# Performance work log

Measured on AMD Instinct MI355X. Metric: run time of the kernel, lower is better.

The kernel has to match this reference:

```python
import jax, jax.numpy as jnp
import numpy as np

V, D, DEPTH, L, H, DH, FF = 32000, 1024, 4, 2048, 16, 64, 4096
INNER = H * DH
EPS = 1e-5


def ln(x, g, b):
    m = jnp.mean(x, axis=-1, keepdims=True)
    v = jnp.mean(jnp.square(x - m), axis=-1, keepdims=True)
    return (x - m) * jax.lax.rsqrt(v + EPS) * g + b


def setup_inputs() -> dict:
    key = jax.random.key(0)
    ks = jax.random.split(key, 16)
    s = 0.02
    inp = {
        'x': jax.random.randint(ks[0], (1, L), 0, V),
        'tok_emb': jax.random.normal(ks[1], (V, D), jnp.float32) * s,
        'pos_emb': jax.random.normal(ks[2], (L, D), jnp.float32) * s,
        'attn_ng': jnp.ones((DEPTH, D), jnp.float32),
        'attn_nb': jnp.zeros((DEPTH, D), jnp.float32),
        'wqkv': jax.random.normal(ks[3], (DEPTH, D, 3 * INNER), jnp.float32) * s,
        'wo': jax.random.normal(ks[4], (DEPTH, INNER, D), jnp.float32) * s,
        'bo': jnp.zeros((DEPTH, D), jnp.float32),
        'out_ng': jnp.ones((DEPTH, D), jnp.float32),
        'out_nb': jnp.zeros((DEPTH, D), jnp.float32),
        'ff_ng': jnp.ones((DEPTH, D), jnp.float32),
        'ff_nb': jnp.zeros((DEPTH, D), jnp.float32),
        'w1': jax.random.normal(ks[5], (DEPTH, D, FF), jnp.float32) * s,
        'b1': jnp.zeros((DEPTH, FF), jnp.float32),
        'w2': jax.random.normal(ks[6], (DEPTH, FF, D), jnp.float32) * s,
        'b2': jnp.zeros((DEPTH, D), jnp.float32),
        'fin_g': jnp.ones((D,), jnp.float32),
        'fin_b': jnp.zeros((D,), jnp.float32),
        'w_logit': jax.random.normal(ks[7], (D, V), jnp.float32) * s,
        'b_logit': jnp.zeros((V,), jnp.float32),
    }
    return inp


def reference(x, tok_emb, pos_emb, attn_ng, attn_nb, wqkv, wo, bo, out_ng, out_nb,
              ff_ng, ff_nb, w1, b1, w2, b2, fin_g, fin_b, w_logit, b_logit):
    n = x.shape[1]
    scale = DH ** -0.5
    # causal keep-mask: j <= i (lower triangular incl diagonal)
    causal = jnp.tril(jnp.ones((n, n), bool))
    h = tok_emb[x] + pos_emb[:n][None]  # [b, n, D]
    for l in range(DEPTH):
        # --- ReLA attention ---
        y = ln(h, attn_ng[l], attn_nb[l])
        qkv = y @ wqkv[l]  # [b, n, 3*INNER]
        q, k, v = jnp.split(qkv, 3, axis=-1)
        q = q.reshape(-1, n, H, DH).transpose(0, 2, 1, 3) * scale  # [b,H,n,d]
        k = k.reshape(-1, n, H, DH).transpose(0, 2, 1, 3)
        v = v.reshape(-1, n, H, DH).transpose(0, 2, 1, 3)
        sim = jnp.einsum('bhid,bhjd->bhij', q, k)
        attn = jnp.where(causal, jax.nn.relu(sim), 0.0)  # mask then ReLU
        o = jnp.einsum('bhij,bhjd->bhid', attn, v)
        o = o.transpose(0, 2, 1, 3).reshape(-1, n, INNER)  # [b,n,INNER]
        o = ln(o @ wo[l] + bo[l], out_ng[l], out_nb[l])
        h = o + h
        # --- FFN ---
        y = ln(h, ff_ng[l], ff_nb[l])
        y = jax.nn.gelu(y @ w1[l] + b1[l], approximate=False) @ w2[l] + b2[l]
        h = y + h
    return ln(h, fin_g, fin_b) @ w_logit + b_logit
```

## Files before the change

kernel.cpp:

```cpp
#include <hip/hip_runtime.h>
#include <hip/hip_bf16.h>
#include <math.h>

#define SEQ   2048
#define DM    1024
#define NH    16
#define DHD   64
#define FFD   4096
#define NV    32000

typedef __bf16 bf16x8 __attribute__((ext_vector_type(8)));
typedef float  f32x4  __attribute__((ext_vector_type(4)));

typedef __attribute__((address_space(1))) void* gas_ptr;
typedef __attribute__((address_space(3))) void* las_ptr;

static __device__ __forceinline__ void gload16(const void* g, void* l) {
  __builtin_amdgcn_global_load_lds((gas_ptr)g, (las_ptr)l, 16, 0, 0);
}

static __device__ __forceinline__ unsigned short f2bf(float f) {
  unsigned int x = __float_as_uint(f);
  return (unsigned short)((x + 0x7fffu + ((x >> 16) & 1u)) >> 16);
}

static __device__ __forceinline__ bf16x8 ld_frag(const unsigned short* p) {
  union { uint4 u; bf16x8 v; } r;
  r.u = *(const uint4*)p;
  return r.v;
}

__global__ __launch_bounds__(256)
void k_transpose_bf16(const float* __restrict__ in, unsigned short* __restrict__ out,
                      int K, int N, size_t lstride) {
  in  += (size_t)blockIdx.z * lstride;
  out += (size_t)blockIdx.z * lstride;
  __shared__ float tl[64 * 65];
  const int bk = blockIdx.x * 64, bn = blockIdx.y * 64;
  const int t = threadIdx.x;
  const int tx = t & 15, ty = t >> 4;
#pragma unroll
  for (int i = 0; i < 4; ++i) {
    const int r = i * 16 + ty;
    float4 v = *(const float4*)&in[(size_t)(bk + r) * N + bn + tx * 4];
    tl[(tx * 4 + 0) * 65 + r] = v.x;
    tl[(tx * 4 + 1) * 65 + r] = v.y;
    tl[(tx * 4 + 2) * 65 + r] = v.z;
    tl[(tx * 4 + 3) * 65 + r] = v.w;
  }
  __syncthreads();
#pragma unroll
  for (int j = 0; j < 2; ++j) {
    const int f = j * 256 + t;
    const int n = f >> 3, kc = (f & 7) * 8;
    union { unsigned short u[8]; uint4 v; } pk;
#pragma unroll
    for (int e = 0; e < 8; ++e) pk.u[e] = f2bf(tl[n * 65 + kc + e]);
    *(uint4*)&out[(size_t)(bn + n) * K + bk + kc] = pk.v;
  }
}

__global__ __launch_bounds__(256)
void k_vT(const unsigned short* __restrict__ qkv, unsigned short* __restrict__ vT) {
  __shared__ unsigned short tile[32][33];
  const int bs = blockIdx.x * 32, bd = blockIdx.y * 32;
  const int tx = threadIdx.x & 31, ty = threadIdx.x >> 5;
#pragma unroll
  for (int r = ty; r < 32; r += 8)
    tile[r][tx] = qkv[(size_t)(bs + r) * (3 * DM) + 2 * DM + bd + tx];
  __syncthreads();
#pragma unroll
  for (int r = ty; r < 32; r += 8)
    vT[(size_t)(bd + r) * SEQ + bs + tx] = tile[tx][r];
}

__global__ __launch_bounds__(256)
void k_embed(const int* __restrict__ x, const float* __restrict__ tok,
             const float* __restrict__ pos, float* __restrict__ h) {
  const int row = blockIdx.x;
  const int d = threadIdx.x * 4;
  const int tk = x[row];
  float4 a = *(const float4*)(tok + (size_t)tk * DM + d);
  float4 p = *(const float4*)(pos + (size_t)row * DM + d);
  float4 o; o.x = a.x + p.x; o.y = a.y + p.y; o.z = a.z + p.z; o.w = a.w + p.w;
  *(float4*)(h + (size_t)row * DM + d) = o;
}

__global__ __launch_bounds__(256)
void k_ln_bf16(const float* __restrict__ in, const float* __restrict__ g,
               const float* __restrict__ b, unsigned short* __restrict__ out) {
  const int row = blockIdx.x, t = threadIdx.x;
  float4 v = *(const float4*)(in + (size_t)row * DM + t * 4);
  float s = v.x + v.y + v.z + v.w;
  float q = v.x * v.x + v.y * v.y + v.z * v.z + v.w * v.w;
#pragma unroll
  for (int o = 32; o; o >>= 1) { s += __shfl_xor(s, o); q += __shfl_xor(q, o); }
  __shared__ float ls[4], lq[4];
  if ((t & 63) == 0) { ls[t >> 6] = s; lq[t >> 6] = q; }
  __syncthreads();
  s = ls[0] + ls[1] + ls[2] + ls[3];
  q = lq[0] + lq[1] + lq[2] + lq[3];
  const float mean = s * (1.f / DM);
  const float rstd = rsqrtf(q * (1.f / DM) - mean * mean + 1e-5f);
  float4 gg = *(const float4*)(g + t * 4);
  float4 bb = *(const float4*)(b + t * 4);
  ushort4 o4;
  o4.x = f2bf((v.x - mean) * rstd * gg.x + bb.x);
  o4.y = f2bf((v.y - mean) * rstd * gg.y + bb.y);
  o4.z = f2bf((v.z - mean) * rstd * gg.z + bb.z);
  o4.w = f2bf((v.w - mean) * rstd * gg.w + bb.w);
  *(ushort4*)(out + (size_t)row * DM + t * 4) = o4;
}

__global__ __launch_bounds__(256)
void k_add_ln_ln(float* __restrict__ h, const float* __restrict__ in,
                 const float* __restrict__ g1, const float* __restrict__ b1,
                 const float* __restrict__ g2, const float* __restrict__ b2,
                 unsigned short* __restrict__ out) {
  const int row = blockIdx.x, t = threadIdx.x;
  __shared__ float ls[4], lq[4], ls2[4], lq2[4];
  float4 v = *(const float4*)(in + (size_t)row * DM + t * 4);
  float s = v.x + v.y + v.z + v.w;
  float q = v.x * v.x + v.y * v.y + v.z * v.z + v.w * v.w;
#pragma unroll
  for (int o = 32; o; o >>= 1) { s += __shfl_xor(s, o); q += __shfl_xor(q, o); }
  if ((t & 63) == 0) { ls[t >> 6] = s; lq[t >> 6] = q; }
  __syncthreads();
  s = ls[0] + ls[1] + ls[2] + ls[3];
  q = lq[0] + lq[1] + lq[2] + lq[3];
  const float mean = s * (1.f / DM);
  const float rstd = rsqrtf(q * (1.f / DM) - mean * mean + 1e-5f);
  float4 gg = *(const float4*)(g1 + t * 4);
  float4 bb = *(const float4*)(b1 + t * 4);
  float4 hv = *(const float4*)(h + (size_t)row * DM + t * 4);
  hv.x += (v.x - mean) * rstd * gg.x + bb.x;
  hv.y += (v.y - mean) * rstd * gg.y + bb.y;
  hv.z += (v.z - mean) * rstd * gg.z + bb.z;
  hv.w += (v.w - mean) * rstd * gg.w + bb.w;
  *(float4*)(h + (size_t)row * DM + t * 4) = hv;
  float s2 = hv.x + hv.y + hv.z + hv.w;
  float q2 = hv.x * hv.x + hv.y * hv.y + hv.z * hv.z + hv.w * hv.w;
#pragma unroll
  for (int o = 32; o; o >>= 1) { s2 += __shfl_xor(s2, o); q2 += __shfl_xor(q2, o); }
  if ((t & 63) == 0) { ls2[t >> 6] = s2; lq2[t >> 6] = q2; }
  __syncthreads();
  s2 = ls2[0] + ls2[1] + ls2[2] + ls2[3];
  q2 = lq2[0] + lq2[1] + lq2[2] + lq2[3];
  const float mean2 = s2 * (1.f / DM);
  const float rstd2 = rsqrtf(q2 * (1.f / DM) - mean2 * mean2 + 1e-5f);
  float4 g2v = *(const float4*)(g2 + t * 4);
  float4 b2v = *(const float4*)(b2 + t * 4);
  ushort4 o4;
  o4.x = f2bf((hv.x - mean2) * rstd2 * g2v.x + b2v.x);
  o4.y = f2bf((hv.y - mean2) * rstd2 * g2v.y + b2v.y);
  o4.z = f2bf((hv.z - mean2) * rstd2 * g2v.z + b2v.z);
  o4.w = f2bf((hv.w - mean2) * rstd2 * g2v.w + b2v.w);
  *(ushort4*)(out + (size_t)row * DM + t * 4) = o4;
}

__global__ __launch_bounds__(256)
void k_red_add(float* __restrict__ h, const float* __restrict__ sl,
               const float* __restrict__ b2) {
  const int row = blockIdx.x, d = threadIdx.x * 4;
  const size_t idx = (size_t)row * DM + d;
  float4 hv = *(const float4*)(h + idx);
  float4 bb = *(const float4*)(b2 + d);
  hv.x += bb.x; hv.y += bb.y; hv.z += bb.z; hv.w += bb.w;
#pragma unroll
  for (int c = 0; c < 4; ++c) {
    float4 p = *(const float4*)(sl + (size_t)c * SEQ * DM + idx);
    hv.x += p.x; hv.y += p.y; hv.z += p.z; hv.w += p.w;
  }
  *(float4*)(h + idx) = hv;
}

template<int EPI>
__global__ __launch_bounds__(512, 1)
void k_gemm2(const unsigned short* __restrict__ A, const unsigned short* __restrict__ Bt,
             float* __restrict__ outF, unsigned short* __restrict__ outB,
             const float* __restrict__ bias, int N, int K, int kLen, int gm) {
  __shared__ __align__(16) unsigned short L[49152];
  const int nwg = gridDim.x, pid = blockIdx.x;
  const int qq = nwg >> 3, rr = nwg & 7;
  const int xcd = pid & 7, lo = pid >> 3;
  const int wg = ((xcd < rr) ? xcd * (qq + 1) : rr * (qq + 1) + (xcd - rr) * qq) + lo;
  const int bm = wg % gm, bn = wg / gm;
  const int kOff = blockIdx.y * kLen;
  const int t = threadIdx.x, lane = t & 63, w = t >> 6;
  const int wm = w >> 2, wn = w & 3, lr = lane & 15, lg = lane >> 4;

  const unsigned short* gA[2]; unsigned short* lA[2];
  const unsigned short* gB[4]; unsigned short* lB[4];
#pragma unroll
  for (int j = 0; j < 2; ++j) {
    const int f = j * 512 + t, row = f >> 3, c = f & 7;
    gA[j] = A + (size_t)(bm * 128 + row) * K + kOff + ((c ^ (row & 7)) << 3);
    lA[j] = L + f * 8;
  }
#pragma unroll
  for (int j = 0; j < 4; ++j) {
    const int f = j * 512 + t, row = f >> 3, c = f & 7;
    gB[j] = Bt + (size_t)(bn * 256 + row) * K + kOff + ((c ^ (row & 7)) << 3);
    lB[j] = L + 16384 + f * 8;
  }
  auto stage = [&](int k0, int c) {
#pragma unroll
    for (int j = 0; j < 2; ++j) gload16(gA[j] + k0, lA[j] + c * 8192);
#pragma unroll
    for (int j = 0; j < 4; ++j) gload16(gB[j] + k0, lB[j] + c * 16384);
  };

  int offA[4][2], offB[4][2];
#pragma unroll
  for (int mt = 0; mt < 4; ++mt)
#pragma unroll
    for (int ks = 0; ks < 2; ++ks) {
      const int rowA = wm * 64 + mt * 16 + lr;
      offA[mt][ks] = rowA * 64 + (((ks * 4 + lg) ^ (rowA & 7)) << 3);
      const int rowB = wn * 64 + mt * 16 + lr;
      offB[mt][ks] = rowB * 64 + (((ks * 4 + lg) ^ (rowB & 7)) << 3);
    }

  const f32x4 zero = {0.f, 0.f, 0.f, 0.f};
  f32x4 acc[4][4];
#pragma unroll
  for (int i = 0; i < 4; ++i)
#pragma unroll
    for (int j = 0; j < 4; ++j) acc[i][j] = zero;

  const int NT = kLen >> 6;
  stage(0, 0);
  if (NT > 1) stage(64, 1);

  for (int tt = 0; tt < NT; ++tt) {
    const int c = tt & 1;
    if (tt + 1 < NT) asm volatile("s_waitcnt vmcnt(6)" ::: "memory");
    else             asm volatile("s_waitcnt vmcnt(0)" ::: "memory");
    __builtin_amdgcn_s_barrier();
    const unsigned short* Ab = L + c * 8192;
    const unsigned short* Bb = L + 16384 + c * 16384;
    bf16x8 af[4][2], bfr[4][2];
#pragma unroll
    for (int mt = 0; mt < 4; ++mt)
#pragma unroll
      for (int ks = 0; ks < 2; ++ks) {
        af[mt][ks]  = ld_frag(Ab + offA[mt][ks]);
        bfr[mt][ks] = ld_frag(Bb + offB[mt][ks]);
      }
    __builtin_amdgcn_s_setprio(1);
#pragma unroll
    for (int mt = 0; mt < 4; ++mt)
#pragma unroll
      for (int nt = 0; nt < 4; ++nt)
#pragma unroll
        for (int ks = 0; ks < 2; ++ks)
          acc[mt][nt] = __builtin_amdgcn_mfma_f32_16x16x32_bf16(af[mt][ks], bfr[nt][ks], acc[mt][nt], 0, 0, 0);
    __builtin_amdgcn_s_setprio(0);
    asm volatile("s_waitcnt lgkmcnt(0)" ::: "memory");
    __builtin_amdgcn_s_barrier();
    if (tt + 2 < NT) stage((tt + 2) << 6, c);
  }

  const int rbase = bm * 128 + wm * 64;
  const int cbase = bn * 256 + wn * 64;
  float* outP = outF;
  if constexpr (EPI == 4) outP = outF + (size_t)blockIdx.y * SEQ * N;
#pragma unroll
  for (int mt = 0; mt < 4; ++mt) {
#pragma unroll
    for (int nt = 0; nt < 4; ++nt) {
      const int col = cbase + nt * 16 + lr;
      float bv = 0.f;
      if constexpr (EPI == 1 || EPI == 2) bv = bias[col];
#pragma unroll
      for (int r = 0; r < 4; ++r) {
        const int row = rbase + mt * 16 + lg * 4 + r;
        float v = acc[mt][nt][r] + bv;
        if constexpr (EPI == 2) v = 0.5f * v * (1.f + erff(v * 0.70710678118f));
        if constexpr (EPI == 0 || EPI == 2) outB[(size_t)row * N + col] = f2bf(v);
        else                                outP[(size_t)row * N + col] = v;
      }
    }
  }
}

__global__ __launch_bounds__(512, 1)
void k_gemm3(const unsigned short* __restrict__ A, const unsigned short* __restrict__ Bt,
             float* __restrict__ outF, const float* __restrict__ bias,
             int N, int K, int gm) {
  __shared__ __align__(16) unsigned short L[65536];
  const int nwg = gridDim.x, pid = blockIdx.x;
  const int qq = nwg >> 3, rr = nwg & 7;
  const int xcd = pid & 7, lo = pid >> 3;
  const int wg = ((xcd < rr) ? xcd * (qq + 1) : rr * (qq + 1) + (xcd - rr) * qq) + lo;
  const int bm = wg % gm, bn = wg / gm;
  const int t = threadIdx.x, lane = t & 63, w = t >> 6;
  const int wm = w >> 2, wn = w & 3, lr = lane & 15, lg = lane >> 4;
  const int NT = K >> 6;

  int offA[8][2], offB[4][2];
#pragma unroll
  for (int mt = 0; mt < 8; ++mt) {
    const int row = mt * 32 + wm * 16 + lr;
#pragma unroll
    for (int ks = 0; ks < 2; ++ks)
      offA[mt][ks] = row * 64 + (((ks * 4 + lg) ^ (row & 7)) << 3);
  }
#pragma unroll
  for (int nt = 0; nt < 4; ++nt) {
    const int row = ((nt & 1) << 6) + ((nt >> 1) << 7) + wn * 16 + lr;
#pragma unroll
    for (int ks = 0; ks < 2; ++ks)
      offB[nt][ks] = 16384 + row * 64 + (((ks * 4 + lg) ^ (row & 7)) << 3);
  }

  const unsigned short* gA = A  + (size_t)(bm * 256) * K;
  const unsigned short* gB = Bt + (size_t)(bn * 256) * K;

  auto stage_half = [&](int which, int tile, int half) {
    const int tt = (tile < NT) ? tile : (NT - 1);
    const unsigned short* g = which ? gB : gA;
    const int bufo = (tile & 1) << 15;
#pragma unroll
    for (int j = 0; j < 2; ++j) {
      const int f = (j << 9) + t;
      const int r = (half << 7) + (f >> 3);
      const int c = (f & 7) ^ (r & 7);
      gload16(g + (size_t)r * K + (tt << 6) + (c << 3),
              L + bufo + (which << 14) + (half << 13) + f * 8);
    }
  };

  f32x4 acc[8][4];
#pragma unroll
  for (int i = 0; i < 8; ++i)
#pragma unroll
    for (int j = 0; j < 4; ++j) acc[i][j] = (f32x4){0.f, 0.f, 0.f, 0.f};
  bf16x8 af[4][2], bfr[2][2];

  stage_half(1, 0, 0); stage_half(0, 0, 1); stage_half(0, 0, 0);
  stage_half(1, 0, 1); stage_half(1, 1, 0); stage_half(0, 1, 1);

#define PHASE(VMS, LDA, LDB, MH, NH, BUFO, SW, ST, SH) do {                    \
  asm volatile("s_waitcnt vmcnt(" VMS ")" ::: "memory");                       \
  __builtin_amdgcn_s_barrier();                                                \
  if (LDA) {                                                                   \
    _Pragma("unroll") for (int mt = 0; mt < 4; ++mt)                           \
    _Pragma("unroll") for (int ks = 0; ks < 2; ++ks)                           \
      af[mt][ks] = ld_frag(L + (BUFO) + offA[(MH) * 4 + mt][ks]);              \
  }                                                                            \
  if (LDB) {                                                                   \
    _Pragma("unroll") for (int n = 0; n < 2; ++n)                              \
    _Pragma("unroll") for (int ks = 0; ks < 2; ++ks)                           \
      bfr[n][ks] = ld_frag(L + (BUFO) + offB[(NH) * 2 + n][ks]);               \
  }                                                                            \
  stage_half((SW), (ST), (SH));                                                \
  asm volatile("s_waitcnt lgkmcnt(0)" ::: "memory");                           \
  __builtin_amdgcn_sched_barrier(0);                                           \
  __builtin_amdgcn_s_setprio(1);                                               \
  _Pragma("unroll") for (int mt = 0; mt < 4; ++mt)                             \
  _Pragma("unroll") for (int n = 0; n < 2; ++n)                                \
  _Pragma("unroll") for (int ks = 0; ks < 2; ++ks)                             \
    acc[(MH) * 4 + mt][(NH) * 2 + n] = __builtin_amdgcn_mfma_f32_16x16x32_bf16(\
        af[mt][ks], bfr[n][ks], acc[(MH) * 4 + mt][(NH) * 2 + n], 0, 0, 0);    \
  __builtin_amdgcn_s_setprio(0);                                               \
} while (0)

  for (int I = 0; I < (NT >> 1); ++I) {
    const int T = I << 1;
    PHASE("4", 1, 1, 0, 0, 0,     0, T + 1, 0);
    PHASE("8", 1, 0, 1, 0, 0,     1, T + 1, 1);
    PHASE("6", 0, 1, 1, 1, 0,     1, T + 2, 0);
    PHASE("8", 1, 0, 0, 1, 0,     0, T + 2, 1);
    PHASE("4", 1, 1, 0, 0, 32768, 0, T + 2, 0);
    PHASE("8", 1, 0, 1, 0, 32768, 1, T + 2, 1);
    PHASE("6", 0, 1, 1, 1, 32768, 1, T + 3, 0);
    PHASE("8", 1, 0, 0, 1, 32768, 0, T + 3, 1);
  }
#undef PHASE

#pragma unroll
  for (int mt = 0; mt < 8; ++mt) {
    const int row0 = bm * 256 + mt * 32 + wm * 16 + lg * 4;
#pragma unroll
    for (int nt = 0; nt < 4; ++nt) {
      const int col = bn * 256 + ((nt & 1) << 6) + ((nt >> 1) << 7) + wn * 16 + lr;
      const float bv = bias[col];
#pragma unroll
      for (int r = 0; r < 4; ++r)
        outF[(size_t)(row0 + r) * N + col] = acc[mt][nt][r] + bv;
    }
  }
}

__global__ __launch_bounds__(256)
void k_rela_attn(const unsigned short* __restrict__ qkv,
                 const unsigned short* __restrict__ vT,
                 unsigned short* __restrict__ obf) {
  const int jb = blockIdx.x;
  const int hd = blockIdx.y;
  const int qbA = jb, qbB = 31 - jb;
  const int t = threadIdx.x, lane = t & 63, w = t >> 6;
  const int lr = lane & 15, lg = lane >> 4;

  __shared__ __align__(16) unsigned short Qs[128 * 64];
  __shared__ __align__(16) unsigned short Ks[64 * 64];
  __shared__ __align__(16) unsigned short Vs[64 * 64];
  __shared__ __align__(16) unsigned short Ps[4][16 * 72];

  const int sr8 = lane >> 3;
  const int sch = ((lane & 7) ^ sr8) << 3;

#pragma unroll
  for (int qi = 0; qi < 4; ++qi) {
    const int i = w * 4 + qi;
    const int rl = i * 8 + sr8;
    const int grow = (rl < 64) ? (qbA * 64 + rl) : (qbB * 64 + rl - 64);
    gload16(qkv + (size_t)grow * (3 * DM) + hd * DHD + sch, Qs + i * 512);
  }
  __syncthreads();

  bf16x8 qfA[2], qfB[2];
#pragma unroll
  for (int ks = 0; ks < 2; ++ks) {
    const int rowA = w * 16 + lr;
    qfA[ks] = ld_frag(&Qs[rowA * 64 + (((ks * 4 + lg) ^ (lr & 7)) << 3)]);
    const int rowB = 64 + w * 16 + lr;
    qfB[ks] = ld_frag(&Qs[rowB * 64 + (((ks * 4 + lg) ^ (lr & 7)) << 3)]);
  }

  const f32x4 zero = {0.f, 0.f, 0.f, 0.f};
  f32x4 accA[4], accB[4];
#pragma unroll
  for (int nt = 0; nt < 4; ++nt) { accA[nt] = zero; accB[nt] = zero; }

  auto tile_step = [&](const bf16x8* qf, f32x4* acc, int qb, int kt) {
    f32x4 sv[4];
#pragma unroll
    for (int nt = 0; nt < 4; ++nt) sv[nt] = zero;
#pragma unroll
    for (int ks = 0; ks < 2; ++ks)
#pragma unroll
      for (int nt = 0; nt < 4; ++nt) {
        bf16x8 kf = ld_frag(&Ks[(nt * 16 + lr) * 64 + (((ks * 4 + lg) ^ (lr & 7)) << 3)]);
        sv[nt] = __builtin_amdgcn_mfma_f32_16x16x32_bf16(qf[ks], kf, sv[nt], 0, 0, 0);
      }
    const bool diag = (kt == qb);
#pragma unroll
    for (int nt = 0; nt < 4; ++nt)
#pragma unroll
      for (int r = 0; r < 4; ++r) {
        float v = fmaxf(sv[nt][r], 0.f) * 0.125f;
        if (diag) {
          const int ii = w * 16 + lg * 4 + r;
          const int jj = nt * 16 + lr;
          if (jj > ii) v = 0.f;
        }
        Ps[w][(lg * 4 + r) * 72 + nt * 16 + lr] = f2bf(v);
      }
#pragma unroll
    for (int ks = 0; ks < 2; ++ks) {
      bf16x8 pf = ld_frag(&Ps[w][lr * 72 + ks * 32 + lg * 8]);
#pragma unroll
      for (int nt = 0; nt < 4; ++nt) {
        bf16x8 vf = ld_frag(&Vs[(nt * 16 + lr) * 64 + (((ks * 4 + lg) ^ (lr & 7)) << 3)]);
        acc[nt] = __builtin_amdgcn_mfma_f32_16x16x32_bf16(pf, vf, acc[nt], 0, 0, 0);
      }
    }
  };

  for (int kt = 0; kt <= qbB; ++kt) {
    __syncthreads();
#pragma unroll
    for (int qi = 0; qi < 2; ++qi) {
      const int i = w * 2 + qi;
      const int rl = i * 8 + sr8;
      gload16(qkv + (size_t)(kt * 64 + rl) * (3 * DM) + DM + hd * DHD + sch, Ks + i * 512);
      gload16(vT + (size_t)(hd * DHD + rl) * SEQ + kt * 64 + sch, Vs + i * 512);
    }
    __syncthreads();
    tile_step(qfB, accB, qbB, kt);
    if (kt <= qbA) tile_step(qfA, accA, qbA, kt);
  }

#pragma unroll
  for (int nt = 0; nt < 4; ++nt)
#pragma unroll
    for (int r = 0; r < 4; ++r) {
      const int col = hd * DHD + nt * 16 + lr;
      const int rowA = qbA * 64 + w * 16 + lg * 4 + r;
      obf[(size_t)rowA * DM + col] = f2bf(accA[nt][r]);
      const int rowB = qbB * 64 + w * 16 + lg * 4 + r;
      obf[(size_t)rowB * DM + col] = f2bf(accB[nt][r]);
    }
}

extern "C" void kernel_launch(void* const* d_in, const int* in_sizes, int n_in,
                              void* d_out, int out_size, void* d_ws, size_t ws_size,
                              hipStream_t stream) {
  const int*   x       = (const int*)d_in[0];
  const float* tok_emb = (const float*)d_in[1];
  const float* pos_emb = (const float*)d_in[2];
  const float* attn_ng = (const float*)d_in[3];
  const float* attn_nb = (const float*)d_in[4];
  const float* wqkv    = (const float*)d_in[5];
  const float* wo      = (const float*)d_in[6];
  const float* bo      = (const float*)d_in[7];
  const float* out_ng  = (const float*)d_in[8];
  const float* out_nb  = (const float*)d_in[9];
  const float* ff_ng   = (const float*)d_in[10];
  const float* ff_nb   = (const float*)d_in[11];
  const float* w1      = (const float*)d_in[12];
  const float* b1      = (const float*)d_in[13];
  const float* w2      = (const float*)d_in[14];
  const float* b2      = (const float*)d_in[15];
  const float* fin_g   = (const float*)d_in[16];
  const float* fin_b   = (const float*)d_in[17];
  const float* w_logit = (const float*)d_in[18];
  const float* b_logit = (const float*)d_in[19];
  float* out = (float*)d_out;

  char* ws = (char*)d_ws;
  size_t off = 0;
  auto alloc = [&](size_t bytes) -> void* {
    void* p = ws + off;
    off = (off + bytes + 255) & ~(size_t)255;
    return p;
  };
  unsigned short* wqkvT = (unsigned short*)alloc(4ull * 3072 * 1024 * 2);
  unsigned short* woT   = (unsigned short*)alloc(4ull * 1024 * 1024 * 2);
  unsigned short* w1T   = (unsigned short*)alloc(4ull * 4096 * 1024 * 2);
  unsigned short* w2T   = (unsigned short*)alloc(4ull * 1024 * 4096 * 2);
  unsigned short* wlogT = (unsigned short*)alloc((size_t)NV * 1024 * 2);
  float*          h     = (float*)alloc((size_t)SEQ * DM * 4);
  unsigned short* ybf   = (unsigned short*)alloc((size_t)SEQ * DM * 2);
  unsigned short* qkvbf = (unsigned short*)alloc((size_t)SEQ * 3 * DM * 2);
  unsigned short* vTb   = (unsigned short*)alloc((size_t)DM * SEQ * 2);
  unsigned short* obf   = (unsigned short*)alloc((size_t)SEQ * DM * 2);
  float*          tmpf  = (float*)alloc((size_t)SEQ * DM * 4);
  unsigned short* ffbf  = (unsigned short*)alloc((size_t)SEQ * FFD * 2);
  float*          slabs = (float*)alloc(4ull * SEQ * DM * 4);
  (void)ws_size; (void)in_sizes; (void)n_in; (void)out_size;

  const dim3 B(256);
  const dim3 G2(512);

  k_transpose_bf16<<<dim3(16, 48, 4), B, 0, stream>>>(wqkv, wqkvT, 1024, 3072, (size_t)1024 * 3072);
  k_transpose_bf16<<<dim3(16, 16, 4), B, 0, stream>>>(wo, woT, 1024, 1024, (size_t)1024 * 1024);
  k_transpose_bf16<<<dim3(16, 64, 4), B, 0, stream>>>(w1, w1T, 1024, 4096, (size_t)1024 * 4096);
  k_transpose_bf16<<<dim3(64, 16, 4), B, 0, stream>>>(w2, w2T, 4096, 1024, (size_t)4096 * 1024);
  k_transpose_bf16<<<dim3(16, 500, 1), B, 0, stream>>>(w_logit, wlogT, 1024, NV, 0);

  k_embed<<<SEQ, B, 0, stream>>>(x, tok_emb, pos_emb, h);

  for (int l = 0; l < 4; ++l) {
    k_ln_bf16<<<SEQ, B, 0, stream>>>(h, attn_ng + l * DM, attn_nb + l * DM, ybf);
    k_gemm2<0><<<dim3(192), G2, 0, stream>>>(
        ybf, wqkvT + (size_t)l * 3072 * 1024, nullptr, qkvbf, nullptr, 3072, 1024, 1024, 16);
    k_vT<<<dim3(SEQ / 32, DM / 32), B, 0, stream>>>(qkvbf, vTb);
    k_rela_attn<<<dim3(16, NH), B, 0, stream>>>(qkvbf, vTb, obf);
    k_gemm2<1><<<dim3(64), G2, 0, stream>>>(
        obf, woT + (size_t)l * 1024 * 1024, tmpf, nullptr, bo + l * DM, 1024, 1024, 1024, 16);
    k_add_ln_ln<<<SEQ, B, 0, stream>>>(h, tmpf, out_ng + l * DM, out_nb + l * DM,
                                       ff_ng + l * DM, ff_nb + l * DM, ybf);
    k_gemm2<2><<<dim3(256), G2, 0, stream>>>(
        ybf, w1T + (size_t)l * 4096 * 1024, nullptr, ffbf, b1 + l * FFD, 4096, 1024, 1024, 16);
    k_gemm2<4><<<dim3(64, 4), G2, 0, stream>>>(
        ffbf, w2T + (size_t)l * 1024 * 4096, slabs, nullptr, nullptr, 1024, 4096, 1024, 16);
    k_red_add<<<SEQ, B, 0, stream>>>(h, slabs, b2 + l * DM);
  }

  k_ln_bf16<<<SEQ, B, 0, stream>>>(h, fin_g, fin_b, ybf);
  k_gemm3<<<dim3(1000), G2, 0, stream>>>(ybf, wlogT, out, b_logit, NV, 1024, 8);
}
```

Measured before the change: 1.140 ms.

## Split-K output projection, reorder gemm2 MFMA loop, simplify logits GEMM pipeline

The output projection GEMM now runs split-K into four slabs, and a new add/LN/LN kernel sums the slabs plus the bias, giving a 256-block grid instead of 64. The gemm2 inner loop is reordered so k-steps are outermost, and an explicit lgkmcnt wait is dropped. The logits GEMM is replaced by a simpler double-buffered kernel with K-tile 32 and half the LDS, and allows higher occupancy via launch bounds. The trade-offs are more slab memory traffic, and a less elaborately phased logits pipeline.

```diff
diff --git a/kernel.cpp b/kernel.cpp
--- a/kernel.cpp
+++ b/kernel.cpp
@@ -113,13 +113,20 @@
 }
 
 __global__ __launch_bounds__(256)
-void k_add_ln_ln(float* __restrict__ h, const float* __restrict__ in,
-                 const float* __restrict__ g1, const float* __restrict__ b1,
-                 const float* __restrict__ g2, const float* __restrict__ b2,
-                 unsigned short* __restrict__ out) {
+void k_addslab_ln_ln(float* __restrict__ h, const float* __restrict__ sl,
+                     const float* __restrict__ bo,
+                     const float* __restrict__ g1, const float* __restrict__ b1,
+                     const float* __restrict__ g2, const float* __restrict__ b2,
+                     unsigned short* __restrict__ out) {
   const int row = blockIdx.x, t = threadIdx.x;
   __shared__ float ls[4], lq[4], ls2[4], lq2[4];
-  float4 v = *(const float4*)(in + (size_t)row * DM + t * 4);
+  const size_t idx = (size_t)row * DM + t * 4;
+  float4 v = *(const float4*)(bo + t * 4);
+#pragma unroll
+  for (int c = 0; c < 4; ++c) {
+    float4 p = *(const float4*)(sl + (size_t)c * SEQ * DM + idx);
+    v.x += p.x; v.y += p.y; v.z += p.z; v.w += p.w;
+  }
   float s = v.x + v.y + v.z + v.w;
   float q = v.x * v.x + v.y * v.y + v.z * v.z + v.w * v.w;
 #pragma unroll
@@ -132,12 +139,12 @@
   const float rstd = rsqrtf(q * (1.f / DM) - mean * mean + 1e-5f);
   float4 gg = *(const float4*)(g1 + t * 4);
   float4 bb = *(const float4*)(b1 + t * 4);
-  float4 hv = *(const float4*)(h + (size_t)row * DM + t * 4);
+  float4 hv = *(const float4*)(h + idx);
   hv.x += (v.x - mean) * rstd * gg.x + bb.x;
   hv.y += (v.y - mean) * rstd * gg.y + bb.y;
   hv.z += (v.z - mean) * rstd * gg.z + bb.z;
   hv.w += (v.w - mean) * rstd * gg.w + bb.w;
-  *(float4*)(h + (size_t)row * DM + t * 4) = hv;
+  *(float4*)(h + idx) = hv;
   float s2 = hv.x + hv.y + hv.z + hv.w;
   float q2 = hv.x * hv.x + hv.y * hv.y + hv.z * hv.z + hv.w * hv.w;
 #pragma unroll
@@ -249,14 +256,13 @@
       }
     __builtin_amdgcn_s_setprio(1);
 #pragma unroll
-    for (int mt = 0; mt < 4; ++mt)
-#pragma unroll
-      for (int nt = 0; nt < 4; ++nt)
-#pragma unroll
-        for (int ks = 0; ks < 2; ++ks)
+    for (int ks = 0; ks < 2; ++ks)
+#pragma unroll
+      for (int mt = 0; mt < 4; ++mt)
+#pragma unroll
+        for (int nt = 0; nt < 4; ++nt)
           acc[mt][nt] = __builtin_amdgcn_mfma_f32_16x16x32_bf16(af[mt][ks], bfr[nt][ks], acc[mt][nt], 0, 0, 0);
     __builtin_amdgcn_s_setprio(0);
-    asm volatile("s_waitcnt lgkmcnt(0)" ::: "memory");
     __builtin_amdgcn_s_barrier();
     if (tt + 2 < NT) stage((tt + 2) << 6, c);
   }
@@ -284,11 +290,11 @@
   }
 }
 
-__global__ __launch_bounds__(512, 1)
-void k_gemm3(const unsigned short* __restrict__ A, const unsigned short* __restrict__ Bt,
+__global__ __launch_bounds__(512, 4)
+void k_gemm5(const unsigned short* __restrict__ A, const unsigned short* __restrict__ Bt,
              float* __restrict__ outF, const float* __restrict__ bias,
              int N, int K, int gm) {
-  __shared__ __align__(16) unsigned short L[65536];
+  __shared__ __align__(16) unsigned short L[32768];
   const int nwg = gridDim.x, pid = blockIdx.x;
   const int qq = nwg >> 3, rr = nwg & 7;
   const int xcd = pid & 7, lo = pid >> 3;
@@ -296,95 +302,75 @@
   const int bm = wg % gm, bn = wg / gm;
   const int t = threadIdx.x, lane = t & 63, w = t >> 6;
   const int wm = w >> 2, wn = w & 3, lr = lane & 15, lg = lane >> 4;
-  const int NT = K >> 6;
-
-  int offA[8][2], offB[4][2];
+
+  const unsigned short* gA[2]; const unsigned short* gB[2];
+  unsigned short* lA[2]; unsigned short* lB[2];
+#pragma unroll
+  for (int j = 0; j < 2; ++j) {
+    const int f = j * 512 + t;
+    const int row = f >> 2, c = (f & 3) ^ (row & 3);
+    gA[j] = A  + (size_t)(bm * 256 + row) * K + c * 8;
+    gB[j] = Bt + (size_t)(bn * 256 + row) * K + c * 8;
+    lA[j] = L + f * 8;
+    lB[j] = L + 8192 + f * 8;
+  }
+  auto stage = [&](int k0, int c) {
+#pragma unroll
+    for (int j = 0; j < 2; ++j) gload16(gA[j] + k0, lA[j] + c * 16384);
+#pragma unroll
+    for (int j = 0; j < 2; ++j) gload16(gB[j] + k0, lB[j] + c * 16384);
+  };
+
+  int offA[8], offB[4];
 #pragma unroll
   for (int mt = 0; mt < 8; ++mt) {
-    const int row = mt * 32 + wm * 16 + lr;
-#pragma unroll
-    for (int ks = 0; ks < 2; ++ks)
-      offA[mt][ks] = row * 64 + (((ks * 4 + lg) ^ (row & 7)) << 3);
+    const int row = wm * 128 + mt * 16 + lr;
+    offA[mt] = row * 32 + ((lg ^ (row & 3)) << 3);
   }
 #pragma unroll
   for (int nt = 0; nt < 4; ++nt) {
-    const int row = ((nt & 1) << 6) + ((nt >> 1) << 7) + wn * 16 + lr;
-#pragma unroll
-    for (int ks = 0; ks < 2; ++ks)
-      offB[nt][ks] = 16384 + row * 64 + (((ks * 4 + lg) ^ (row & 7)) << 3);
-  }
-
-  const unsigned short* gA = A  + (size_t)(bm * 256) * K;
-  const unsigned short* gB = Bt + (size_t)(bn * 256) * K;
-
-  auto stage_half = [&](int which, int tile, int half) {
-    const int tt = (tile < NT) ? tile : (NT - 1);
-    const unsigned short* g = which ? gB : gA;
-    const int bufo = (tile & 1) << 15;
-#pragma unroll
-    for (int j = 0; j < 2; ++j) {
-      const int f = (j << 9) + t;
-      const int r = (half << 7) + (f >> 3);
-      const int c = (f & 7) ^ (r & 7);
-      gload16(g + (size_t)r * K + (tt << 6) + (c << 3),
-              L + bufo + (which << 14) + (half << 13) + f * 8);
-    }
-  };
+    const int row = wn * 64 + nt * 16 + lr;
+    offB[nt] = 8192 + row * 32 + ((lg ^ (row & 3)) << 3);
+  }
 
   f32x4 acc[8][4];
 #pragma unroll
   for (int i = 0; i < 8; ++i)
 #pragma unroll
     for (int j = 0; j < 4; ++j) acc[i][j] = (f32x4){0.f, 0.f, 0.f, 0.f};
-  bf16x8 af[4][2], bfr[2][2];
-
-  stage_half(1, 0, 0); stage_half(0, 0, 1); stage_half(0, 0, 0);
-  stage_half(1, 0, 1); stage_half(1, 1, 0); stage_half(0, 1, 1);
-
-#define PHASE(VMS, LDA, LDB, MH, NH, BUFO, SW, ST, SH) do {                    \
-  asm volatile("s_waitcnt vmcnt(" VMS ")" ::: "memory");                       \
-  __builtin_amdgcn_s_barrier();                                                \
-  if (LDA) {                                                                   \
-    _Pragma("unroll") for (int mt = 0; mt < 4; ++mt)                           \
-    _Pragma("unroll") for (int ks = 0; ks < 2; ++ks)                           \
-      af[mt][ks] = ld_frag(L + (BUFO) + offA[(MH) * 4 + mt][ks]);              \
-  }                                                                            \
-  if (LDB) {                                                                   \
-    _Pragma("unroll") for (int n = 0; n < 2; ++n)                              \
-    _Pragma("unroll") for (int ks = 0; ks < 2; ++ks)                           \
-      bfr[n][ks] = ld_frag(L + (BUFO) + offB[(NH) * 2 + n][ks]);               \
-  }                                                                            \
-  stage_half((SW), (ST), (SH));                                                \
-  asm volatile("s_waitcnt lgkmcnt(0)" ::: "memory");                           \
-  __builtin_amdgcn_sched_barrier(0);                                           \
-  __builtin_amdgcn_s_setprio(1);                                               \
-  _Pragma("unroll") for (int mt = 0; mt < 4; ++mt)                             \
-  _Pragma("unroll") for (int n = 0; n < 2; ++n)                                \
-  _Pragma("unroll") for (int ks = 0; ks < 2; ++ks)                             \
-    acc[(MH) * 4 + mt][(NH) * 2 + n] = __builtin_amdgcn_mfma_f32_16x16x32_bf16(\
-        af[mt][ks], bfr[n][ks], acc[(MH) * 4 + mt][(NH) * 2 + n], 0, 0, 0);    \
-  __builtin_amdgcn_s_setprio(0);                                               \
-} while (0)
-
-  for (int I = 0; I < (NT >> 1); ++I) {
-    const int T = I << 1;
-    PHASE("4", 1, 1, 0, 0, 0,     0, T + 1, 0);
-    PHASE("8", 1, 0, 1, 0, 0,     1, T + 1, 1);
-    PHASE("6", 0, 1, 1, 1, 0,     1, T + 2, 0);
-    PHASE("8", 1, 0, 0, 1, 0,     0, T + 2, 1);
-    PHASE("4", 1, 1, 0, 0, 32768, 0, T + 2, 0);
-    PHASE("8", 1, 0, 1, 0, 32768, 1, T + 2, 1);
-    PHASE("6", 0, 1, 1, 1, 32768, 1, T + 3, 0);
-    PHASE("8", 1, 0, 0, 1, 32768, 0, T + 3, 1);
-  }
-#undef PHASE
+
+  const int NT = K >> 5;
+  stage(0, 0);
+  stage(32, 1);
+
+  for (int tt = 0; tt < NT; ++tt) {
+    const int c = tt & 1;
+    if (tt + 1 < NT) asm volatile("s_waitcnt vmcnt(4)" ::: "memory");
+    else             asm volatile("s_waitcnt vmcnt(0)" ::: "memory");
+    __builtin_amdgcn_s_barrier();
+    const unsigned short* buf = L + c * 16384;
+    bf16x8 bfr[4];
+#pragma unroll
+    for (int nt = 0; nt < 4; ++nt) bfr[nt] = ld_frag(buf + offB[nt]);
+    __builtin_amdgcn_s_setprio(1);
+#pragma unroll
+    for (int mt = 0; mt < 8; ++mt) {
+      bf16x8 af = ld_frag(buf + offA[mt]);
+#pragma unroll
+      for (int nt = 0; nt < 4; ++nt)
+        acc[mt][nt] = __builtin_amdgcn_mfma_f32_16x16x32_bf16(af, bfr[nt], acc[mt][nt], 0, 0, 0);
+    }
+    __builtin_amdgcn_s_setprio(0);
+    __builtin_amdgcn_s_barrier();
+    if (tt + 2 < NT) stage((tt + 2) << 5, c);
+  }
 
 #pragma unroll
   for (int mt = 0; mt < 8; ++mt) {
-    const int row0 = bm * 256 + mt * 32 + wm * 16 + lg * 4;
+    const int row0 = bm * 256 + wm * 128 + mt * 16 + lg * 4;
 #pragma unroll
     for (int nt = 0; nt < 4; ++nt) {
-      const int col = bn * 256 + ((nt & 1) << 6) + ((nt >> 1) << 7) + wn * 16 + lr;
+      const int col = bn * 256 + wn * 64 + nt * 16 + lr;
       const float bv = bias[col];
 #pragma unroll
       for (int r = 0; r < 4; ++r)
@@ -540,7 +526,7 @@
   float*          tmpf  = (float*)alloc((size_t)SEQ * DM * 4);
   unsigned short* ffbf  = (unsigned short*)alloc((size_t)SEQ * FFD * 2);
   float*          slabs = (float*)alloc(4ull * SEQ * DM * 4);
-  (void)ws_size; (void)in_sizes; (void)n_in; (void)out_size;
+  (void)ws_size; (void)in_sizes; (void)n_in; (void)out_size; (void)tmpf;
 
   const dim3 B(256);
   const dim3 G2(512);
@@ -559,10 +545,11 @@
         ybf, wqkvT + (size_t)l * 3072 * 1024, nullptr, qkvbf, nullptr, 3072, 1024, 1024, 16);
     k_vT<<<dim3(SEQ / 32, DM / 32), B, 0, stream>>>(qkvbf, vTb);
     k_rela_attn<<<dim3(16, NH), B, 0, stream>>>(qkvbf, vTb, obf);
-    k_gemm2<1><<<dim3(64), G2, 0, stream>>>(
-        obf, woT + (size_t)l * 1024 * 1024, tmpf, nullptr, bo + l * DM, 1024, 1024, 1024, 16);
-    k_add_ln_ln<<<SEQ, B, 0, stream>>>(h, tmpf, out_ng + l * DM, out_nb + l * DM,
-                                       ff_ng + l * DM, ff_nb + l * DM, ybf);
+    k_gemm2<4><<<dim3(64, 4), G2, 0, stream>>>(
+        obf, woT + (size_t)l * 1024 * 1024, slabs, nullptr, nullptr, 1024, 1024, 256, 16);
+    k_addslab_ln_ln<<<SEQ, B, 0, stream>>>(h, slabs, bo + l * DM,
+                                           out_ng + l * DM, out_nb + l * DM,
+                                           ff_ng + l * DM, ff_nb + l * DM, ybf);
     k_gemm2<2><<<dim3(256), G2, 0, stream>>>(
         ybf, w1T + (size_t)l * 4096 * 1024, nullptr, ffbf, b1 + l * FFD, 4096, 1024, 1024, 16);
     k_gemm2<4><<<dim3(64, 4), G2, 0, stream>>>(
@@ -571,5 +558,5 @@
   }
 
   k_ln_bf16<<<SEQ, B, 0, stream>>>(h, fin_g, fin_b, ybf);
-  k_gemm3<<<dim3(1000), G2, 0, stream>>>(ybf, wlogT, out, b_logit, NV, 1024, 8);
-}
+  k_gemm5<<<dim3(1000), G2, 0, stream>>>(ybf, wlogT, out, b_logit, NV, 1024, 8);
+}
```

Result: slower. 1.702 ms (+49.3%).
